# Kernel tuning notes

Hardware: AMD Instinct MI355X
Metric: run time of the kernel (lower is better)

## Reference

```python
import jax, jax.numpy as jnp
import numpy as np

HEIGHT = 8
IN_DIM = 128
OUT_DIM = 8
BATCH = 65536
INT_NODES = 2 ** HEIGHT - 1   # 255
LEAF_NODES = 2 ** HEIGHT      # 256


def _and_weight(height):
    # Fixed +-1 structured routing matrix [leaf, int_nodes] (DGTreg._get_and_layer_params).
    leaf = 2 ** height
    w = np.zeros((leaf, leaf - 1), dtype=np.float32)
    for i in range(height):
        num = 2 ** i
        start = num - 1
        for j in range(start, start + num):
            rb = leaf // num * (j - start)
            rm = rb + leaf // (2 * num)
            re = rb + leaf // num
            w[rb:rm, j] = 1.0
            w[rm:re, j] = -1.0
    return jnp.asarray(w)


def setup_inputs() -> dict:
    key = jax.random.key(0)
    k = jax.random.split(key, 5)
    x = jax.random.normal(k[0], (BATCH, IN_DIM), jnp.float32)
    # orthogonal-ish predicate weight (scaled gaussian), zero bias per module init
    Wp = jax.random.normal(k[1], (INT_NODES, IN_DIM), jnp.float32) / np.sqrt(IN_DIM)
    bp = jnp.zeros((INT_NODES,), jnp.float32)
    Wand = _and_weight(HEIGHT)
    # xavier_uniform for or-layer weights [out_dim, in_dim, leaf]
    lim = np.sqrt(6.0 / (IN_DIM + LEAF_NODES)).astype(np.float32)
    Wor = jax.random.uniform(k[2], (OUT_DIM, IN_DIM, LEAF_NODES), jnp.float32, -lim, lim)
    bor = jax.random.normal(k[3], (OUT_DIM, IN_DIM), jnp.float32) * 0.01
    lim2 = np.sqrt(6.0 / (LEAF_NODES + OUT_DIM)).astype(np.float32)
    action_stds = jax.random.uniform(k[4], (LEAF_NODES, OUT_DIM), jnp.float32, -lim2, lim2)
    return {"x": x, "Wp": Wp, "bp": bp, "Wand": Wand, "Wor": Wor, "bor": bor,
            "action_stds": action_stds}


def reference(x, Wp, bp, Wand, Wor, bor, action_stds):
    sg = jax.lax.stop_gradient
    # predicate layer: [B, int_nodes]
    pred_z = x @ Wp.T + bp
    # ScaleBinarizer1: fac = mean(|z|) per row; binarize to {fac, 0}; straight-through grad
    fac = jnp.mean(jnp.abs(pred_z), axis=-1, keepdims=True)
    binz = jnp.where(pred_z >= 0, fac, 0.0)
    pred_a = pred_z + sg(binz - pred_z)          # forward = binz, grad = identity
    pred_a = 2.0 * pred_a - sg(fac)              # in {+fac, -fac}
    # fixed structured 'and' layer -> softmax over leaves
    and_z = pred_a @ Wand.T                      # [B, leaf]
    and_a = jax.nn.softmax(and_z, axis=-1)
    # Sparser1: keep only max entry per row, straight-through grad
    mx = jnp.max(and_a, axis=-1, keepdims=True)
    sp = jnp.where(and_a >= mx, and_a, 0.0)
    and_a = and_a + sg(sp - and_a)
    # or layers: per-output Linear(leaf->in_dim) then <wt, x>
    wt = jnp.einsum('bl,oil->boi', and_a, Wor) + bor[None]   # [B, out, in]
    out = jnp.einsum('boi,bi->bo', wt, x)                    # [B, out]
    # std head over detached routing weights
    std = jnp.sum(action_stds[None] * sg(and_a)[:, :, None], axis=1)  # [B, out]
    std = jnp.clip(std, -20.0, 2.0)
    return (out, std)
```

## Files before the change

kernel.cpp:

```cpp
#include <hip/hip_runtime.h>

#define BATCH 65536
#define IN_DIM 128
#define INT_NODES 255
#define LEAF 256
#define OUT_DIM 8
#define AMB_TH 4e-3f

typedef float    f4v __attribute__((ext_vector_type(4)));
typedef _Float16 h8v __attribute__((ext_vector_type(8)));

__global__ __launch_bounds__(256) void prep(const float* __restrict__ Wor,
                                            float* __restrict__ Wor_t,
                                            const float* __restrict__ Wp,
                                            _Float16* __restrict__ Bf) {
    if (blockIdx.x < 64) {
        __shared__ float t[64][65];
        const int rt = blockIdx.x >> 2, ct = blockIdx.x & 3;
        const int r0 = rt * 64, c0 = ct * 64;
        const int tx = threadIdx.x & 63, ty = threadIdx.x >> 6;
#pragma unroll
        for (int p = 0; p < 16; ++p) {
            int r = ty + p * 4;
            t[r][tx] = Wor[(size_t)(r0 + r) * 256 + c0 + tx];
        }
        __syncthreads();
#pragma unroll
        for (int p = 0; p < 16; ++p) {
            int r = ty + p * 4;
            Wor_t[(size_t)(c0 + r) * 1024 + r0 + tx] = t[tx][r];
        }
    } else {
        int slot = (blockIdx.x - 64) * 256 + threadIdx.x;
        int j    = slot & 7;
        int lane = (slot >> 3) & 63;
        int ntg  = (slot >> 9) & 15;
        int ks   = slot >> 13;
        int n = ntg * 16 + (lane & 15);
        int k = ks * 32 + (lane >> 4) * 8 + j;
        float v = (n < INT_NODES) ? Wp[n * IN_DIM + k] : 0.f;
        Bf[slot] = (_Float16)v;
    }
}

__global__ __launch_bounds__(256) void dgt_main(
    const float* __restrict__ x, const float* __restrict__ Wp,
    const float* __restrict__ bp, const _Float16* __restrict__ Bfg,
    const float* __restrict__ Wor_t, const float* __restrict__ bor,
    const float* __restrict__ stds,
    float* __restrict__ out, float* __restrict__ stdo) {

    __shared__ unsigned char sgn[LEAF * 16];
    __shared__ float P[64 * 68];
    __shared__ float S[256];
    __shared__ float H[64 * 33];
    __shared__ float psL[64];
    __shared__ int   leafL[64];

    const int tid  = threadIdx.x;
    const int wave = tid >> 6;
    const int lane = tid & 63;
    const int c = lane & 15;
    const int g = lane >> 4;
    const int rowbase = blockIdx.x * 64;

    f4v acc[4][4];
#pragma unroll
    for (int mt = 0; mt < 4; ++mt)
#pragma unroll
        for (int nt = 0; nt < 4; ++nt) acc[mt][nt] = (f4v){0.f, 0.f, 0.f, 0.f};

    const h8v* Bf8 = (const h8v*)Bfg;
    const float* xbase = x + (size_t)rowbase * IN_DIM;
#pragma unroll
    for (int ks = 0; ks < 4; ++ks) {
        h8v ah[4];
#pragma unroll
        for (int mt = 0; mt < 4; ++mt) {
            const float* p = xbase + (size_t)(mt * 16 + c) * IN_DIM + ks * 32 + g * 8;
            float4 v0 = *reinterpret_cast<const float4*>(p);
            float4 v1 = *reinterpret_cast<const float4*>(p + 4);
            h8v a;
            a[0] = (_Float16)v0.x; a[1] = (_Float16)v0.y;
            a[2] = (_Float16)v0.z; a[3] = (_Float16)v0.w;
            a[4] = (_Float16)v1.x; a[5] = (_Float16)v1.y;
            a[6] = (_Float16)v1.z; a[7] = (_Float16)v1.w;
            ah[mt] = a;
        }
#pragma unroll
        for (int nt = 0; nt < 4; ++nt) {
            h8v b = Bf8[(ks * 16 + (wave * 4 + nt)) * 64 + lane];
#pragma unroll
            for (int mt = 0; mt < 4; ++mt)
                acc[mt][nt] = __builtin_amdgcn_mfma_f32_16x16x32_f16(ah[mt], b, acc[mt][nt], 0, 0, 0);
        }
    }

    {
        float pp[4][4];
#pragma unroll
        for (int mt = 0; mt < 4; ++mt)
#pragma unroll
            for (int rr = 0; rr < 4; ++rr) pp[mt][rr] = 0.f;
#pragma unroll
        for (int nt = 0; nt < 4; ++nt) {
            const int n = wave * 64 + nt * 16 + c;
            const float bpv = (n < INT_NODES) ? bp[n] : 0.f;
#pragma unroll
            for (int mt = 0; mt < 4; ++mt) {
                unsigned by = 0;
#pragma unroll
                for (int rr = 0; rr < 4; ++rr) {
                    float v = acc[mt][nt][rr] + bpv;
                    float av = fabsf(v);
                    if (n < INT_NODES) pp[mt][rr] += av;
                    by |= ((v < 0.f ? 1u : 0u) | (av < AMB_TH ? 2u : 0u)) << (2 * rr);
                }
                sgn[n * 16 + mt * 4 + g] = (unsigned char)by;
            }
        }
#pragma unroll
        for (int mt = 0; mt < 4; ++mt)
#pragma unroll
            for (int rr = 0; rr < 4; ++rr)
                P[(wave * 16 + c) * 68 + mt * 16 + g * 4 + rr] = pp[mt][rr];
    }
    __syncthreads();

    {
        const int r = tid & 63, q = tid >> 6;
        float s = 0.f;
#pragma unroll
        for (int cc = 0; cc < 16; ++cc) s += P[(q * 16 + cc) * 68 + r];
        S[q * 64 + r] = s;
    }
    __syncthreads();

    {
        const int r = tid >> 2, kq = tid & 3;
        float asum = S[r] + S[64 + r] + S[128 + r] + S[192 + r];
        const float fac = asum * (1.0f / (float)INT_NODES);
        const float e = expf(-2.0f * fac);
        const float qq = 1.0f + e;
        const float q2 = qq * qq, q4 = q2 * q2, q8 = q4 * q4;
        const float ps = 1.0f / q8;

        int node = 0;
#pragma unroll
        for (int d = 0; d < 8; ++d) {
            unsigned by = sgn[node * 16 + (r >> 2)];
            int code = (int)((by >> ((r & 3) * 2)) & 3u);
            int neg;
            if (code & 2) {
                double zd = (double)bp[node];
                const float* wr = Wp + node * IN_DIM;
                const float* xrow = x + (size_t)(rowbase + r) * IN_DIM;
                for (int k = 0; k < IN_DIM; ++k)
                    zd = fma((double)wr[k], (double)xrow[k], zd);
                neg = (zd < 0.0) ? 1 : 0;
            } else {
                neg = code & 1;
            }
            node = 2 * node + 1 + neg;
        }
        const int leaf = node - INT_NODES;
        if (kq == 0) { psL[r] = ps; leafL[r] = leaf; }

        const float* xr = x + (size_t)(rowbase + r) * IN_DIM;
        const float* wl = Wor_t + (size_t)leaf * 1024;
        float hp[8];
#pragma unroll
        for (int o = 0; o < 8; ++o) hp[o] = 0.f;
        float tp[8];
#pragma unroll
        for (int o = 0; o < 8; ++o) tp[o] = 0.f;
#pragma unroll
        for (int step = 0; step < 8; ++step) {
            const int off = (step * 4 + kq) * 4;
            float4 xv = *reinterpret_cast<const float4*>(xr + off);
#pragma unroll
            for (int o = 0; o < 8; ++o) {
                float4 wv = *reinterpret_cast<const float4*>(wl + o * IN_DIM + off);
                float4 bv = *reinterpret_cast<const float4*>(bor + o * IN_DIM + off);
                hp[o] = fmaf(wv.x, xv.x, hp[o]); hp[o] = fmaf(wv.y, xv.y, hp[o]);
                hp[o] = fmaf(wv.z, xv.z, hp[o]); hp[o] = fmaf(wv.w, xv.w, hp[o]);
                tp[o] = fmaf(bv.x, xv.x, tp[o]); tp[o] = fmaf(bv.y, xv.y, tp[o]);
                tp[o] = fmaf(bv.z, xv.z, tp[o]); tp[o] = fmaf(bv.w, xv.w, tp[o]);
            }
        }
#pragma unroll
        for (int o = 0; o < 8; ++o)
            H[r * 33 + o * 4 + kq] = ps * hp[o] + tp[o];
    }
    __syncthreads();

    {
        const int r = tid & 63, p = tid >> 6;
        const float ps = psL[r];
        const int leaf = leafL[r];
#pragma unroll
        for (int u = 0; u < 2; ++u) {
            const int o = p * 2 + u;
            float v = H[r * 33 + o * 4 + 0] + H[r * 33 + o * 4 + 1]
                    + H[r * 33 + o * 4 + 2] + H[r * 33 + o * 4 + 3];
            out[(size_t)(rowbase + r) * OUT_DIM + o] = v;
            float sd = ps * stds[leaf * OUT_DIM + o];
            stdo[(size_t)(rowbase + r) * OUT_DIM + o] = fminf(fmaxf(sd, -20.0f), 2.0f);
        }
    }
}

extern "C" void kernel_launch(void* const* d_in, const int* in_sizes, int n_in,
                              void* d_out, int out_size, void* d_ws, size_t ws_size,
                              hipStream_t stream) {
    const float* x    = (const float*)d_in[0];
    const float* Wp   = (const float*)d_in[1];
    const float* bp   = (const float*)d_in[2];
    const float* Wor  = (const float*)d_in[4];
    const float* bor  = (const float*)d_in[5];
    const float* stds = (const float*)d_in[6];
    float* out = (float*)d_out;

    char* ws = (char*)d_ws;
    float* wor_t = (float*)(ws);
    _Float16* Bf = (_Float16*)(ws + (1 << 20));

    prep<<<192, 256, 0, stream>>>(Wor, wor_t, Wp, Bf);
    dgt_main<<<BATCH / 64, 256, 0, stream>>>(x, Wp, bp, Bf, wor_t, bor, stds,
                                             out, out + (size_t)BATCH * OUT_DIM);
}
```

Before: 132.3 us.

## Halve rows per block to 32 and split or-layer dot across 8 lanes

Each block now handles 32 batch rows instead of 64, so twice as many blocks launch, with fewer MFMA accumulators and registers per thread. The predicate GEMM keeps the same B fragments but uses two M-tiles. Phase 3 now gives 8 threads per row instead of 4, and the partial-sum reduction and shared buffers are resized to match. The aim is more parallelism and occupancy, and a shorter serial tree walk and or-layer dot product per thread. In exchange, each block reloads the full Bf weight fragments for half as many rows.

```diff
diff --git a/kernel.cpp b/kernel.cpp
--- a/kernel.cpp
+++ b/kernel.cpp
@@ -5,6 +5,8 @@
 #define INT_NODES 255
 #define LEAF 256
 #define OUT_DIM 8
+#define ROWS_PB 32
+#define NBLK (BATCH / ROWS_PB)
 #define AMB_TH 4e-3f
 
 typedef float    f4v __attribute__((ext_vector_type(4)));
@@ -50,23 +52,23 @@
     const float* __restrict__ stds,
     float* __restrict__ out, float* __restrict__ stdo) {
 
-    __shared__ unsigned char sgn[LEAF * 16];
-    __shared__ float P[64 * 68];
-    __shared__ float S[256];
-    __shared__ float H[64 * 33];
-    __shared__ float psL[64];
-    __shared__ int   leafL[64];
+    __shared__ unsigned char sgn[LEAF * 8];
+    __shared__ float P[64 * 36];
+    __shared__ float S[8 * 32];
+    __shared__ float H[32 * 68];
+    __shared__ float psL[32];
+    __shared__ int   leafL[32];
 
     const int tid  = threadIdx.x;
     const int wave = tid >> 6;
     const int lane = tid & 63;
     const int c = lane & 15;
     const int g = lane >> 4;
-    const int rowbase = blockIdx.x * 64;
-
-    f4v acc[4][4];
-#pragma unroll
-    for (int mt = 0; mt < 4; ++mt)
+    const int rowbase = blockIdx.x * ROWS_PB;
+
+    f4v acc[2][4];
+#pragma unroll
+    for (int mt = 0; mt < 2; ++mt)
 #pragma unroll
         for (int nt = 0; nt < 4; ++nt) acc[mt][nt] = (f4v){0.f, 0.f, 0.f, 0.f};
 
@@ -74,9 +76,9 @@
     const float* xbase = x + (size_t)rowbase * IN_DIM;
 #pragma unroll
     for (int ks = 0; ks < 4; ++ks) {
-        h8v ah[4];
-#pragma unroll
-        for (int mt = 0; mt < 4; ++mt) {
+        h8v ah[2];
+#pragma unroll
+        for (int mt = 0; mt < 2; ++mt) {
             const float* p = xbase + (size_t)(mt * 16 + c) * IN_DIM + ks * 32 + g * 8;
             float4 v0 = *reinterpret_cast<const float4*>(p);
             float4 v1 = *reinterpret_cast<const float4*>(p + 4);
@@ -91,15 +93,15 @@
         for (int nt = 0; nt < 4; ++nt) {
             h8v b = Bf8[(ks * 16 + (wave * 4 + nt)) * 64 + lane];
 #pragma unroll
-            for (int mt = 0; mt < 4; ++mt)
+            for (int mt = 0; mt < 2; ++mt)
                 acc[mt][nt] = __builtin_amdgcn_mfma_f32_16x16x32_f16(ah[mt], b, acc[mt][nt], 0, 0, 0);
         }
     }
 
     {
-        float pp[4][4];
-#pragma unroll
-        for (int mt = 0; mt < 4; ++mt)
+        float pp[2][4];
+#pragma unroll
+        for (int mt = 0; mt < 2; ++mt)
 #pragma unroll
             for (int rr = 0; rr < 4; ++rr) pp[mt][rr] = 0.f;
 #pragma unroll
@@ -107,7 +109,7 @@
             const int n = wave * 64 + nt * 16 + c;
             const float bpv = (n < INT_NODES) ? bp[n] : 0.f;
 #pragma unroll
-            for (int mt = 0; mt < 4; ++mt) {
+            for (int mt = 0; mt < 2; ++mt) {
                 unsigned by = 0;
 #pragma unroll
                 for (int rr = 0; rr < 4; ++rr) {
@@ -116,29 +118,31 @@
                     if (n < INT_NODES) pp[mt][rr] += av;
                     by |= ((v < 0.f ? 1u : 0u) | (av < AMB_TH ? 2u : 0u)) << (2 * rr);
                 }
-                sgn[n * 16 + mt * 4 + g] = (unsigned char)by;
+                sgn[n * 8 + mt * 4 + g] = (unsigned char)by;
             }
         }
 #pragma unroll
-        for (int mt = 0; mt < 4; ++mt)
+        for (int mt = 0; mt < 2; ++mt)
 #pragma unroll
             for (int rr = 0; rr < 4; ++rr)
-                P[(wave * 16 + c) * 68 + mt * 16 + g * 4 + rr] = pp[mt][rr];
+                P[(wave * 16 + c) * 36 + mt * 16 + g * 4 + rr] = pp[mt][rr];
     }
     __syncthreads();
 
     {
-        const int r = tid & 63, q = tid >> 6;
+        const int r = tid & 31, q = tid >> 5;
         float s = 0.f;
 #pragma unroll
-        for (int cc = 0; cc < 16; ++cc) s += P[(q * 16 + cc) * 68 + r];
-        S[q * 64 + r] = s;
+        for (int cc = 0; cc < 8; ++cc) s += P[(q * 8 + cc) * 36 + r];
+        S[q * 32 + r] = s;
     }
     __syncthreads();
 
     {
-        const int r = tid >> 2, kq = tid & 3;
-        float asum = S[r] + S[64 + r] + S[128 + r] + S[192 + r];
+        const int r = tid >> 3, kq = tid & 7;
+        float asum = 0.f;
+#pragma unroll
+        for (int j = 0; j < 8; ++j) asum += S[j * 32 + r];
         const float fac = asum * (1.0f / (float)INT_NODES);
         const float e = expf(-2.0f * fac);
         const float qq = 1.0f + e;
@@ -148,7 +152,7 @@
         int node = 0;
 #pragma unroll
         for (int d = 0; d < 8; ++d) {
-            unsigned by = sgn[node * 16 + (r >> 2)];
+            unsigned by = sgn[node * 8 + (r >> 2)];
             int code = (int)((by >> ((r & 3) * 2)) & 3u);
             int neg;
             if (code & 2) {
@@ -168,15 +172,12 @@
 
         const float* xr = x + (size_t)(rowbase + r) * IN_DIM;
         const float* wl = Wor_t + (size_t)leaf * 1024;
-        float hp[8];
-#pragma unroll
-        for (int o = 0; o < 8; ++o) hp[o] = 0.f;
-        float tp[8];
-#pragma unroll
-        for (int o = 0; o < 8; ++o) tp[o] = 0.f;
-#pragma unroll
-        for (int step = 0; step < 8; ++step) {
-            const int off = (step * 4 + kq) * 4;
+        float hp[8], tp[8];
+#pragma unroll
+        for (int o = 0; o < 8; ++o) { hp[o] = 0.f; tp[o] = 0.f; }
+#pragma unroll
+        for (int step = 0; step < 4; ++step) {
+            const int off = (step * 8 + kq) * 4;
             float4 xv = *reinterpret_cast<const float4*>(xr + off);
 #pragma unroll
             for (int o = 0; o < 8; ++o) {
@@ -190,23 +191,17 @@
         }
 #pragma unroll
         for (int o = 0; o < 8; ++o)
-            H[r * 33 + o * 4 + kq] = ps * hp[o] + tp[o];
+            H[r * 68 + o * 8 + kq] = ps * hp[o] + tp[o];
     }
     __syncthreads();
 
     {
-        const int r = tid & 63, p = tid >> 6;
-        const float ps = psL[r];
-        const int leaf = leafL[r];
-#pragma unroll
-        for (int u = 0; u < 2; ++u) {
-            const int o = p * 2 + u;
-            float v = H[r * 33 + o * 4 + 0] + H[r * 33 + o * 4 + 1]
-                    + H[r * 33 + o * 4 + 2] + H[r * 33 + o * 4 + 3];
-            out[(size_t)(rowbase + r) * OUT_DIM + o] = v;
-            float sd = ps * stds[leaf * OUT_DIM + o];
-            stdo[(size_t)(rowbase + r) * OUT_DIM + o] = fminf(fmaxf(sd, -20.0f), 2.0f);
-        }
+        const int r = tid & 31, o = tid >> 5;
+        const float* h = &H[r * 68 + o * 8];
+        float v = ((h[0] + h[1]) + (h[2] + h[3])) + ((h[4] + h[5]) + (h[6] + h[7]));
+        out[(size_t)(rowbase + r) * OUT_DIM + o] = v;
+        float sd = psL[r] * stds[leafL[r] * OUT_DIM + o];
+        stdo[(size_t)(rowbase + r) * OUT_DIM + o] = fminf(fmaxf(sd, -20.0f), 2.0f);
     }
 }
 
@@ -226,6 +221,6 @@
     _Float16* Bf = (_Float16*)(ws + (1 << 20));
 
     prep<<<192, 256, 0, stream>>>(Wor, wor_t, Wp, Bf);
-    dgt_main<<<BATCH / 64, 256, 0, stream>>>(x, Wp, bp, Bf, wor_t, bor, stds,
-                                             out, out + (size_t)BATCH * OUT_DIM);
+    dgt_main<<<NBLK, 256, 0, stream>>>(x, Wp, bp, Bf, wor_t, bor, stds,
+                                       out, out + (size_t)BATCH * OUT_DIM);
 }
```

Result: slower. 136.5 us (+3.2%).
